# Optimization experiments

Measured on AMD Instinct MI355X. Metric: run time of the kernel, lower is better.

Reference implementation:

```python
import jax, jax.numpy as jnp
import numpy as np

B, T, H, M = 64, 1024, 512, 256  # batch, max_time, out_dim(=annot_dim), memory_dim


def setup_inputs() -> dict:
    key = jax.random.key(0)
    ks = jax.random.split(key, 13)
    s = lambda k, shape, scale=1.0: jax.random.normal(k, shape, dtype=jnp.float32) * scale
    return {
        "memory": s(ks[0], (B, M)),
        "context": s(ks[1], (B, H)),
        "rnn_state": s(ks[2], (B, H)),
        "annotations": s(ks[3], (B, T, H)),
        "W_ih": s(ks[4], (3 * H, H + M), 0.04),
        "b_ih": s(ks[5], (3 * H,), 0.04),
        "W_hh": s(ks[6], (3 * H, H), 0.04),
        "b_hh": s(ks[7], (3 * H,), 0.04),
        "Wq": s(ks[8], (H, H), 0.04),
        "bq": s(ks[9], (H,), 0.04),
        "Wa": s(ks[10], (H, H), 0.04),
        "ba": s(ks[11], (H,), 0.04),
        "v": s(ks[12], (H,), 0.04),
    }


def reference(memory, context, rnn_state, annotations,
              W_ih, b_ih, W_hh, b_hh, Wq, bq, Wa, ba, v):
    # --- GRUCell step (torch semantics) ---
    x = jnp.concatenate([memory, context], axis=-1)          # (B, M+H)
    gi = x @ W_ih.T + b_ih                                   # (B, 3H)
    gh = rnn_state @ W_hh.T + b_hh                           # (B, 3H)
    i_r, i_z, i_n = jnp.split(gi, 3, axis=-1)
    h_r, h_z, h_n = jnp.split(gh, 3, axis=-1)
    r = jax.nn.sigmoid(i_r + h_r)
    z = jax.nn.sigmoid(i_z + h_z)
    n = jnp.tanh(i_n + r * h_n)
    h_new = (1.0 - z) * n + z * rnn_state                    # (B, H)

    # --- Bahdanau additive attention ---
    pq = h_new @ Wq.T + bq                                   # (B, H)
    pa = annotations @ Wa.T + ba                             # (B, T, H)
    scores = jnp.tanh(pq[:, None, :] + pa) @ v               # (B, T)
    align = jax.nn.softmax(scores, axis=-1)                  # (B, T)
    ctx = jnp.einsum('bt,btd->bd', align, annotations)       # (B, H)
    return (h_new, ctx, align)
```

## Files before the change

kernel.cpp:

```cpp
#include <hip/hip_runtime.h>
#include <hip/hip_bf16.h>


typedef __attribute__((ext_vector_type(8))) __bf16 bf16x8;
typedef __attribute__((ext_vector_type(8))) unsigned short u16x8;
typedef __attribute__((ext_vector_type(4))) float f32x4;
typedef __attribute__((ext_vector_type(4))) float f4v;

__device__ __forceinline__ unsigned short f2bf(float f) {
    __hip_bfloat16 h = __float2bfloat16(f);
    return __builtin_bit_cast(unsigned short, h);
}
__device__ __forceinline__ float tanh_fast(float x) {
    float e = __expf(2.0f * x);
    return 1.0f - 2.0f / (e + 1.0f);
}
__device__ __forceinline__ float sigmoid_f(float x) {
    return 1.0f / (1.0f + __expf(-x));
}
__device__ __forceinline__ int swz(int x) { return x ^ (((x >> 8) & 7) << 4); }
__device__ __forceinline__ f4v ntload4(const float* p) {
    return __builtin_nontemporal_load((const f4v*)p);
}

__global__ __launch_bounds__(256) void wconv_kernel(
    const float* __restrict__ W_ih, const float* __restrict__ W_hh,
    const float* __restrict__ Wq, const float* __restrict__ Wa,
    unsigned short* __restrict__ WihB, unsigned short* __restrict__ WhhB,
    unsigned short* __restrict__ WqB, unsigned short* __restrict__ WaB)
{
    const int cb = blockIdx.x * 4 + (threadIdx.x >> 6);
    const int l = threadIdx.x & 63;
    const float* src;
    unsigned short* dst;
    int K, local, NB, kt;
    if (cb < 2304) {
        src = W_ih; dst = WihB; K = 768; local = cb;
        NB = local / 24; kt = local % 24;
    } else if (cb < 3840) {
        src = W_hh; dst = WhhB; K = 512; local = cb - 2304;
        NB = local >> 4; kt = local & 15;
    } else if (cb < 4352) {
        src = Wq; dst = WqB; K = 512; local = cb - 3840;
        NB = local >> 4; kt = local & 15;
    } else {
        src = Wa; dst = WaB; K = 512; local = cb - 4352;
        NB = local >> 4; kt = local & 15;
    }
    const float* s = src + (size_t)(NB * 16 + (l & 15)) * K + kt * 32 + (l >> 4) * 8;
    float4 f0 = *(const float4*)s;
    float4 f1 = *(const float4*)(s + 4);
    u16x8 p;
    p[0] = f2bf(f0.x); p[1] = f2bf(f0.y); p[2] = f2bf(f0.z); p[3] = f2bf(f0.w);
    p[4] = f2bf(f1.x); p[5] = f2bf(f1.y); p[6] = f2bf(f1.z); p[7] = f2bf(f1.w);
    *(u16x8*)&dst[(size_t)local * 512 + l * 8] = p;
}

#define CVT8(f0, f1, AF)                                                           \
    {                                                                              \
        u16x8 p_;                                                                  \
        p_[0] = f2bf((f0).x); p_[1] = f2bf((f0).y); p_[2] = f2bf((f0).z); p_[3] = f2bf((f0).w); \
        p_[4] = f2bf((f1).x); p_[5] = f2bf((f1).y); p_[6] = f2bf((f1).z); p_[7] = f2bf((f1).w); \
        AF = __builtin_bit_cast(bf16x8, p_);                                       \
    }

__global__ __launch_bounds__(64) void gru_kernel(
    const float* __restrict__ memory, const float* __restrict__ context,
    const float* __restrict__ rnn_state,
    const unsigned short* __restrict__ WihB, const float* __restrict__ b_ih,
    const unsigned short* __restrict__ WhhB, const float* __restrict__ b_hh,
    float* __restrict__ h_new)
{
    const int l = threadIdx.x;
    const int mt = blockIdx.x >> 5;
    const int hb = blockIdx.x & 31;
    const int r = l & 15, g = l >> 4;
    const int row = mt * 16 + r;

    f32x4 a_ir = {0,0,0,0}, a_iz = {0,0,0,0}, a_in = {0,0,0,0};
    f32x4 a_hr = {0,0,0,0}, a_hz = {0,0,0,0}, a_hn = {0,0,0,0};

#pragma unroll
    for (int kt = 0; kt < 8; ++kt) {
        const float* s = memory + (size_t)row * 256 + kt * 32 + g * 8;
        float4 f0 = *(const float4*)s, f1 = *(const float4*)(s + 4);
        bf16x8 af; CVT8(f0, f1, af);
        bf16x8 b0 = __builtin_bit_cast(bf16x8, *(const u16x8*)&WihB[((size_t)(hb) * 24 + kt) * 512 + l * 8]);
        bf16x8 b1 = __builtin_bit_cast(bf16x8, *(const u16x8*)&WihB[((size_t)(32 + hb) * 24 + kt) * 512 + l * 8]);
        bf16x8 b2 = __builtin_bit_cast(bf16x8, *(const u16x8*)&WihB[((size_t)(64 + hb) * 24 + kt) * 512 + l * 8]);
        a_ir = __builtin_amdgcn_mfma_f32_16x16x32_bf16(af, b0, a_ir, 0, 0, 0);
        a_iz = __builtin_amdgcn_mfma_f32_16x16x32_bf16(af, b1, a_iz, 0, 0, 0);
        a_in = __builtin_amdgcn_mfma_f32_16x16x32_bf16(af, b2, a_in, 0, 0, 0);
    }
#pragma unroll
    for (int kt = 8; kt < 24; ++kt) {
        const float* s = context + (size_t)row * 512 + (kt - 8) * 32 + g * 8;
        float4 f0 = *(const float4*)s, f1 = *(const float4*)(s + 4);
        bf16x8 af; CVT8(f0, f1, af);
        bf16x8 b0 = __builtin_bit_cast(bf16x8, *(const u16x8*)&WihB[((size_t)(hb) * 24 + kt) * 512 + l * 8]);
        bf16x8 b1 = __builtin_bit_cast(bf16x8, *(const u16x8*)&WihB[((size_t)(32 + hb) * 24 + kt) * 512 + l * 8]);
        bf16x8 b2 = __builtin_bit_cast(bf16x8, *(const u16x8*)&WihB[((size_t)(64 + hb) * 24 + kt) * 512 + l * 8]);
        a_ir = __builtin_amdgcn_mfma_f32_16x16x32_bf16(af, b0, a_ir, 0, 0, 0);
        a_iz = __builtin_amdgcn_mfma_f32_16x16x32_bf16(af, b1, a_iz, 0, 0, 0);
        a_in = __builtin_amdgcn_mfma_f32_16x16x32_bf16(af, b2, a_in, 0, 0, 0);
    }
#pragma unroll
    for (int kt = 0; kt < 16; ++kt) {
        const float* s = rnn_state + (size_t)row * 512 + kt * 32 + g * 8;
        float4 f0 = *(const float4*)s, f1 = *(const float4*)(s + 4);
        bf16x8 af; CVT8(f0, f1, af);
        bf16x8 b0 = __builtin_bit_cast(bf16x8, *(const u16x8*)&WhhB[((size_t)(hb) * 16 + kt) * 512 + l * 8]);
        bf16x8 b1 = __builtin_bit_cast(bf16x8, *(const u16x8*)&WhhB[((size_t)(32 + hb) * 16 + kt) * 512 + l * 8]);
        bf16x8 b2 = __builtin_bit_cast(bf16x8, *(const u16x8*)&WhhB[((size_t)(64 + hb) * 16 + kt) * 512 + l * 8]);
        a_hr = __builtin_amdgcn_mfma_f32_16x16x32_bf16(af, b0, a_hr, 0, 0, 0);
        a_hz = __builtin_amdgcn_mfma_f32_16x16x32_bf16(af, b1, a_hz, 0, 0, 0);
        a_hn = __builtin_amdgcn_mfma_f32_16x16x32_bf16(af, b2, a_hn, 0, 0, 0);
    }
    const int c = hb * 16 + r;
    const float bir = b_ih[c], biz = b_ih[512 + c], bin = b_ih[1024 + c];
    const float bhr = b_hh[c], bhz = b_hh[512 + c], bhn = b_hh[1024 + c];
#pragma unroll
    for (int r2 = 0; r2 < 4; ++r2) {
        const int m = mt * 16 + g * 4 + r2;
        float rr = sigmoid_f(a_ir[r2] + bir + a_hr[r2] + bhr);
        float zz = sigmoid_f(a_iz[r2] + biz + a_hz[r2] + bhz);
        float nn = tanh_fast(a_in[r2] + bin + rr * (a_hn[r2] + bhn));
        float h0 = rnn_state[(size_t)m * 512 + c];
        h_new[(size_t)m * 512 + c] = (1.f - zz) * nn + zz * h0;
    }
}

__global__ __launch_bounds__(64) void pq_kernel(
    const float* __restrict__ h_new, const unsigned short* __restrict__ WqB,
    const float* __restrict__ bq, const float* __restrict__ ba,
    float* __restrict__ q)
{
    const int l = threadIdx.x;
    const int mt = blockIdx.x >> 5;
    const int hb = blockIdx.x & 31;
    const int r = l & 15, g = l >> 4;
    const int row = mt * 16 + r;
    f32x4 acc = {0,0,0,0};
#pragma unroll
    for (int kt = 0; kt < 16; ++kt) {
        const float* s = h_new + (size_t)row * 512 + kt * 32 + g * 8;
        float4 f0 = *(const float4*)s, f1 = *(const float4*)(s + 4);
        bf16x8 af; CVT8(f0, f1, af);
        bf16x8 b0 = __builtin_bit_cast(bf16x8, *(const u16x8*)&WqB[((size_t)hb * 16 + kt) * 512 + l * 8]);
        acc = __builtin_amdgcn_mfma_f32_16x16x32_bf16(af, b0, acc, 0, 0, 0);
    }
    const int c = hb * 16 + r;
    const float add = bq[c] + ba[c];
#pragma unroll
    for (int r2 = 0; r2 < 4; ++r2)
        q[(size_t)(mt * 16 + g * 4 + r2) * 512 + c] = acc[r2] + add;
}

__global__ __launch_bounds__(512, 2) void scores_kernel(
    const float* __restrict__ ann, const unsigned short* __restrict__ WaB,
    const float* __restrict__ qv, const float* __restrict__ v,
    float* __restrict__ scores)
{
    __shared__ unsigned short As[65536];
    __shared__ float s_sc[128];
    const int tid = threadIdx.x;
    const int l = tid & 63;
    const int w = tid >> 6;
    const int wr = w >> 2;
    const int wc = w & 3;
    const int r0 = blockIdx.x * 128;
    const int b = blockIdx.x >> 3;

    if (tid < 128) s_sc[tid] = 0.f;

#pragma unroll
    for (int p = 0; p < 16; ++p) {
        int cidx = tid + p * 512;
        int row = cidx >> 6;
        int c8 = cidx & 63;
        int kt = c8 >> 2, g = c8 & 3;
        int rtg = row >> 4, r15 = row & 15;
        const float* s = ann + (size_t)(r0 + row) * 512 + c8 * 8;
        f4v f0 = ntload4(s);
        f4v f1 = ntload4(s + 4);
        u16x8 pk;
        pk[0] = f2bf(f0[0]); pk[1] = f2bf(f0[1]); pk[2] = f2bf(f0[2]); pk[3] = f2bf(f0[3]);
        pk[4] = f2bf(f1[0]); pk[5] = f2bf(f1[1]); pk[6] = f2bf(f1[2]); pk[7] = f2bf(f1[3]);
        int logical = (((rtg * 16 + kt) * 64) + g * 16 + r15) * 16;
        *(u16x8*)((char*)As + swz(logical)) = pk;
    }
    __syncthreads();

    f32x4 acc[4][8];
#pragma unroll
    for (int i = 0; i < 4; ++i)
#pragma unroll
        for (int j = 0; j < 8; ++j) acc[i][j] = (f32x4){0.f, 0.f, 0.f, 0.f};

#define LOADB(BV, ktv)                                                                 \
    {                                                                                  \
        _Pragma("unroll")                                                              \
        for (int ct_ = 0; ct_ < 8; ++ct_)                                              \
            BV[ct_] = *(const u16x8*)(WaB +                                            \
                ((size_t)((wc * 8 + ct_) * 16 + (ktv))) * 512 + l * 8);                \
    }

#define MFMA_K(ktv, BV)                                                                \
    {                                                                                  \
        _Pragma("unroll")                                                              \
        for (int rt_ = 0; rt_ < 4; ++rt_) {                                            \
            int logical = (((wr * 4 + rt_) * 16 + (ktv)) * 64 + l) * 16;               \
            bf16x8 af_ = __builtin_bit_cast(bf16x8,                                    \
                *(const u16x8*)((char*)As + swz(logical)));                            \
            _Pragma("unroll")                                                          \
            for (int ct_ = 0; ct_ < 8; ++ct_)                                          \
                acc[rt_][ct_] = __builtin_amdgcn_mfma_f32_16x16x32_bf16(               \
                    af_, __builtin_bit_cast(bf16x8, BV[ct_]), acc[rt_][ct_], 0, 0, 0); \
        }                                                                              \
    }

    u16x8 bvE[8], bvO[8];
    LOADB(bvE, 0);
    for (int kt2 = 0; kt2 < 8; ++kt2) {
        LOADB(bvO, 2 * kt2 + 1);
        MFMA_K(2 * kt2, bvE);
        if (kt2 < 7) LOADB(bvE, 2 * kt2 + 2);
        MFMA_K(2 * kt2 + 1, bvO);
    }
#undef LOADB
#undef MFMA_K

    float rsum[4][4];
#pragma unroll
    for (int i = 0; i < 4; ++i)
#pragma unroll
        for (int j = 0; j < 4; ++j) rsum[i][j] = 0.f;

#pragma unroll
    for (int ct = 0; ct < 8; ++ct) {
        int col = wc * 128 + ct * 16 + (l & 15);
        float qq = qv[b * 512 + col];
        float vv = v[col];
#pragma unroll
        for (int rt = 0; rt < 4; ++rt) {
            f32x4 a = acc[rt][ct];
#pragma unroll
            for (int r2 = 0; r2 < 4; ++r2)
                rsum[rt][r2] += tanh_fast(a[r2] + qq) * vv;
        }
    }
#pragma unroll
    for (int m = 1; m < 16; m <<= 1) {
#pragma unroll
        for (int rt = 0; rt < 4; ++rt)
#pragma unroll
            for (int r2 = 0; r2 < 4; ++r2)
                rsum[rt][r2] += __shfl_xor(rsum[rt][r2], m, 64);
    }
    if ((l & 15) == 0) {
        int g = l >> 4;
#pragma unroll
        for (int rt = 0; rt < 4; ++rt)
#pragma unroll
            for (int r2 = 0; r2 < 4; ++r2)
                atomicAdd(&s_sc[wr * 64 + rt * 16 + g * 4 + r2], rsum[rt][r2]);
    }
    __syncthreads();
    if (tid < 128) scores[r0 + tid] = s_sc[tid];
}

__global__ __launch_bounds__(256) void softmax_kernel(
    const float* __restrict__ scores, float* __restrict__ align_)
{
    const int b = blockIdx.x, tid = threadIdx.x;
    __shared__ float red[256];
    float s[4];
#pragma unroll
    for (int j = 0; j < 4; ++j) s[j] = scores[b * 1024 + j * 256 + tid];
    float mx = fmaxf(fmaxf(s[0], s[1]), fmaxf(s[2], s[3]));
    red[tid] = mx; __syncthreads();
    for (int off = 128; off > 0; off >>= 1) {
        if (tid < off) red[tid] = fmaxf(red[tid], red[tid + off]);
        __syncthreads();
    }
    mx = red[0]; __syncthreads();
    float e[4], sum = 0.f;
#pragma unroll
    for (int j = 0; j < 4; ++j) { e[j] = __expf(s[j] - mx); sum += e[j]; }
    red[tid] = sum; __syncthreads();
    for (int off = 128; off > 0; off >>= 1) {
        if (tid < off) red[tid] += red[tid + off];
        __syncthreads();
    }
    float inv = 1.0f / red[0];
#pragma unroll
    for (int j = 0; j < 4; ++j) align_[b * 1024 + j * 256 + tid] = e[j] * inv;
}

__global__ __launch_bounds__(256) void ctx_part_kernel(
    const float* __restrict__ ann, const float* __restrict__ align_,
    float* __restrict__ part)
{
    const int tid = threadIdx.x;
    const int b = blockIdx.x;
    const int tc = blockIdx.y;
    __shared__ float al[128];
    __shared__ float4 red[128];
    if (tid < 128) al[tid] = align_[b * 1024 + tc * 128 + tid];
    __syncthreads();
    const int rp = tid >> 7, d4 = (tid & 127) * 4;
    const float* ap = ann + ((size_t)(b * 1024 + tc * 128)) * 512 + d4;
    float4 acc = {0.f, 0.f, 0.f, 0.f};
    for (int tt = rp; tt < 128; tt += 2) {
        float4 x = *(const float4*)(ap + (size_t)tt * 512);
        float wv = al[tt];
        acc.x += wv * x.x; acc.y += wv * x.y; acc.z += wv * x.z; acc.w += wv * x.w;
    }
    if (rp == 1) red[tid & 127] = acc;
    __syncthreads();
    if (rp == 0) {
        float4 o = red[tid];
        o.x += acc.x; o.y += acc.y; o.z += acc.z; o.w += acc.w;
        *(float4*)&part[((size_t)(tc * 64 + b)) * 512 + d4] = o;
    }
}

__global__ __launch_bounds__(256) void ctx_reduce_kernel(
    const float* __restrict__ part, float* __restrict__ ctx)
{
    int i4 = (blockIdx.x * 256 + threadIdx.x) * 4;
    float4 s = {0.f, 0.f, 0.f, 0.f};
#pragma unroll
    for (int p = 0; p < 8; ++p) {
        float4 x = *(const float4*)&part[(size_t)p * 32768 + i4];
        s.x += x.x; s.y += x.y; s.z += x.z; s.w += x.w;
    }
    *(float4*)&ctx[i4] = s;
}

extern "C" void kernel_launch(void* const* d_in, const int* in_sizes, int n_in,
                              void* d_out, int out_size, void* d_ws, size_t ws_size,
                              hipStream_t stream)
{
    (void)in_sizes; (void)n_in; (void)out_size; (void)ws_size;
    const float* memory    = (const float*)d_in[0];
    const float* context   = (const float*)d_in[1];
    const float* rnn_state = (const float*)d_in[2];
    const float* ann       = (const float*)d_in[3];
    const float* W_ih      = (const float*)d_in[4];
    const float* b_ih      = (const float*)d_in[5];
    const float* W_hh      = (const float*)d_in[6];
    const float* b_hh      = (const float*)d_in[7];
    const float* Wq        = (const float*)d_in[8];
    const float* bq        = (const float*)d_in[9];
    const float* Wa        = (const float*)d_in[10];
    const float* ba        = (const float*)d_in[11];
    const float* v         = (const float*)d_in[12];

    float* out    = (float*)d_out;
    float* h_new  = out;
    float* ctx    = out + 32768;
    float* align_ = out + 65536;

    char* wsb = (char*)d_ws;
    float* q    = (float*)(wsb + 0);
    float* sc   = (float*)(wsb + 131072);
    float* part = (float*)(wsb + 393216);
    unsigned short* WihB = (unsigned short*)(wsb + 1441792);
    unsigned short* WhhB = (unsigned short*)(wsb + 3801088);
    unsigned short* WqB  = (unsigned short*)(wsb + 5373952);
    unsigned short* WaB  = (unsigned short*)(wsb + 5898240);

    wconv_kernel<<<dim3(1216), dim3(256), 0, stream>>>(
        W_ih, W_hh, Wq, Wa, WihB, WhhB, WqB, WaB);
    gru_kernel<<<dim3(128), dim3(64), 0, stream>>>(
        memory, context, rnn_state, WihB, b_ih, WhhB, b_hh, h_new);
    pq_kernel<<<dim3(128), dim3(64), 0, stream>>>(h_new, WqB, bq, ba, q);
    scores_kernel<<<dim3(512), dim3(512), 0, stream>>>(ann, WaB, q, v, sc);
    softmax_kernel<<<dim3(64), dim3(256), 0, stream>>>(sc, align_);
    ctx_part_kernel<<<dim3(64, 8), dim3(256), 0, stream>>>(ann, align_, part);
    ctx_reduce_kernel<<<dim3(32), dim3(256), 0, stream>>>(part, ctx);
}
```

Baseline: 130.2 us.

## Stage Wa slice in LDS and stream annotations from registers in scores kernel

The scores kernel now splits the output columns into four 128-column slices per block. Each block loads its Wa slice into LDS once with global_load_lds, and each wave streams its 64 annotation rows directly from global memory into registers, converting them to bf16 on the fly. Partial scores for each column slice go to a 4x workspace buffer, and the softmax kernel adds them up, which replaces the shared-memory atomics. The cost is that annotations are read four times, once per column slice, in exchange for Wa staying resident in LDS. The grid also shrinks to 256 blocks, each handling two 512-row passes.

```diff
diff --git a/kernel.cpp b/kernel.cpp
--- a/kernel.cpp
+++ b/kernel.cpp
@@ -5,7 +5,6 @@
 typedef __attribute__((ext_vector_type(8))) __bf16 bf16x8;
 typedef __attribute__((ext_vector_type(8))) unsigned short u16x8;
 typedef __attribute__((ext_vector_type(4))) float f32x4;
-typedef __attribute__((ext_vector_type(4))) float f4v;
 
 __device__ __forceinline__ unsigned short f2bf(float f) {
     __hip_bfloat16 h = __float2bfloat16(f);
@@ -17,10 +16,6 @@
 }
 __device__ __forceinline__ float sigmoid_f(float x) {
     return 1.0f / (1.0f + __expf(-x));
-}
-__device__ __forceinline__ int swz(int x) { return x ^ (((x >> 8) & 7) << 4); }
-__device__ __forceinline__ f4v ntload4(const float* p) {
-    return __builtin_nontemporal_load((const f4v*)p);
 }
 
 __global__ __launch_bounds__(256) void wconv_kernel(
@@ -159,124 +154,123 @@
 __global__ __launch_bounds__(512, 2) void scores_kernel(
     const float* __restrict__ ann, const unsigned short* __restrict__ WaB,
     const float* __restrict__ qv, const float* __restrict__ v,
-    float* __restrict__ scores)
-{
-    __shared__ unsigned short As[65536];
-    __shared__ float s_sc[128];
+    float* __restrict__ sc4)
+{
+    __shared__ unsigned short Bs[65536];
     const int tid = threadIdx.x;
     const int l = tid & 63;
     const int w = tid >> 6;
-    const int wr = w >> 2;
-    const int wc = w & 3;
-    const int r0 = blockIdx.x * 128;
-    const int b = blockIdx.x >> 3;
-
-    if (tid < 128) s_sc[tid] = 0.f;
+    const int bid = blockIdx.x;
+    const int cs = (bid >> 3) & 3;
+    const int rg = ((bid >> 5) << 3) | (bid & 7);
 
 #pragma unroll
     for (int p = 0; p < 16; ++p) {
-        int cidx = tid + p * 512;
-        int row = cidx >> 6;
-        int c8 = cidx & 63;
-        int kt = c8 >> 2, g = c8 & 3;
-        int rtg = row >> 4, r15 = row & 15;
-        const float* s = ann + (size_t)(r0 + row) * 512 + c8 * 8;
-        f4v f0 = ntload4(s);
-        f4v f1 = ntload4(s + 4);
-        u16x8 pk;
-        pk[0] = f2bf(f0[0]); pk[1] = f2bf(f0[1]); pk[2] = f2bf(f0[2]); pk[3] = f2bf(f0[3]);
-        pk[4] = f2bf(f1[0]); pk[5] = f2bf(f1[1]); pk[6] = f2bf(f1[2]); pk[7] = f2bf(f1[3]);
-        int logical = (((rtg * 16 + kt) * 64) + g * 16 + r15) * 16;
-        *(u16x8*)((char*)As + swz(logical)) = pk;
+        int chunk = w + p * 8;
+        const unsigned short* gsrc =
+            WaB + ((size_t)((cs * 8 + (chunk >> 4)) * 16 + (chunk & 15))) * 512 + l * 8;
+        unsigned short* ldst = &Bs[chunk * 512 + l * 8];
+        __builtin_amdgcn_global_load_lds(
+            (const __attribute__((address_space(1))) unsigned int*)gsrc,
+            (__attribute__((address_space(3))) unsigned int*)ldst, 16, 0, 0);
     }
     __syncthreads();
 
-    f32x4 acc[4][8];
-#pragma unroll
-    for (int i = 0; i < 4; ++i)
-#pragma unroll
-        for (int j = 0; j < 8; ++j) acc[i][j] = (f32x4){0.f, 0.f, 0.f, 0.f};
-
-#define LOADB(BV, ktv)                                                                 \
-    {                                                                                  \
-        _Pragma("unroll")                                                              \
-        for (int ct_ = 0; ct_ < 8; ++ct_)                                              \
-            BV[ct_] = *(const u16x8*)(WaB +                                            \
-                ((size_t)((wc * 8 + ct_) * 16 + (ktv))) * 512 + l * 8);                \
-    }
-
-#define MFMA_K(ktv, BV)                                                                \
+#define LOADA(AR, ktv)                                                                 \
     {                                                                                  \
         _Pragma("unroll")                                                              \
         for (int rt_ = 0; rt_ < 4; ++rt_) {                                            \
-            int logical = (((wr * 4 + rt_) * 16 + (ktv)) * 64 + l) * 16;               \
-            bf16x8 af_ = __builtin_bit_cast(bf16x8,                                    \
-                *(const u16x8*)((char*)As + swz(logical)));                            \
+            const float* s_ = abase + (size_t)rt_ * (16 * 512) + (ktv) * 32;           \
+            AR[rt_][0] = *(const float4*)s_;                                           \
+            AR[rt_][1] = *(const float4*)(s_ + 4);                                     \
+        }                                                                              \
+    }
+
+#define MFMA_K(AR, ktv)                                                                \
+    {                                                                                  \
+        _Pragma("unroll")                                                              \
+        for (int rt_ = 0; rt_ < 4; ++rt_) {                                            \
+            bf16x8 af_; CVT8(AR[rt_][0], AR[rt_][1], af_);                             \
             _Pragma("unroll")                                                          \
-            for (int ct_ = 0; ct_ < 8; ++ct_)                                          \
+            for (int ct_ = 0; ct_ < 8; ++ct_) {                                        \
+                bf16x8 bf_ = __builtin_bit_cast(bf16x8,                                \
+                    *(const u16x8*)&Bs[(ct_ * 16 + (ktv)) * 512 + l * 8]);             \
                 acc[rt_][ct_] = __builtin_amdgcn_mfma_f32_16x16x32_bf16(               \
-                    af_, __builtin_bit_cast(bf16x8, BV[ct_]), acc[rt_][ct_], 0, 0, 0); \
+                    af_, bf_, acc[rt_][ct_], 0, 0, 0);                                 \
+            }                                                                          \
         }                                                                              \
     }
 
-    u16x8 bvE[8], bvO[8];
-    LOADB(bvE, 0);
-    for (int kt2 = 0; kt2 < 8; ++kt2) {
-        LOADB(bvO, 2 * kt2 + 1);
-        MFMA_K(2 * kt2, bvE);
-        if (kt2 < 7) LOADB(bvE, 2 * kt2 + 2);
-        MFMA_K(2 * kt2 + 1, bvO);
-    }
-#undef LOADB
+    for (int p2 = 0; p2 < 2; ++p2) {
+        const int row_base = rg * 1024 + p2 * 512 + w * 64;
+        const float* abase = ann + (size_t)(row_base + (l & 15)) * 512 + (l >> 4) * 8;
+
+        f32x4 acc[4][8];
+#pragma unroll
+        for (int i = 0; i < 4; ++i)
+#pragma unroll
+            for (int j = 0; j < 8; ++j) acc[i][j] = (f32x4){0.f, 0.f, 0.f, 0.f};
+
+        float4 aE[4][2], aO[4][2];
+        LOADA(aE, 0);
+        for (int kt2 = 0; kt2 < 8; ++kt2) {
+            LOADA(aO, 2 * kt2 + 1);
+            MFMA_K(aE, 2 * kt2);
+            if (kt2 < 7) LOADA(aE, 2 * kt2 + 2);
+            MFMA_K(aO, 2 * kt2 + 1);
+        }
+
+        float rsum[4][4];
+#pragma unroll
+        for (int i = 0; i < 4; ++i)
+#pragma unroll
+            for (int j = 0; j < 4; ++j) rsum[i][j] = 0.f;
+
+#pragma unroll
+        for (int ct = 0; ct < 8; ++ct) {
+            int col = cs * 128 + ct * 16 + (l & 15);
+            float qq = qv[rg * 512 + col];
+            float vv = v[col];
+#pragma unroll
+            for (int rt = 0; rt < 4; ++rt) {
+                f32x4 a = acc[rt][ct];
+#pragma unroll
+                for (int r2 = 0; r2 < 4; ++r2)
+                    rsum[rt][r2] += tanh_fast(a[r2] + qq) * vv;
+            }
+        }
+#pragma unroll
+        for (int m = 1; m < 16; m <<= 1) {
+#pragma unroll
+            for (int rt = 0; rt < 4; ++rt)
+#pragma unroll
+                for (int r2 = 0; r2 < 4; ++r2)
+                    rsum[rt][r2] += __shfl_xor(rsum[rt][r2], m, 64);
+        }
+        if ((l & 15) == 0) {
+            int g = l >> 4;
+#pragma unroll
+            for (int rt = 0; rt < 4; ++rt)
+#pragma unroll
+                for (int r2 = 0; r2 < 4; ++r2)
+                    sc4[(size_t)cs * 65536 + row_base + rt * 16 + g * 4 + r2] = rsum[rt][r2];
+        }
+    }
+#undef LOADA
 #undef MFMA_K
-
-    float rsum[4][4];
-#pragma unroll
-    for (int i = 0; i < 4; ++i)
-#pragma unroll
-        for (int j = 0; j < 4; ++j) rsum[i][j] = 0.f;
-
-#pragma unroll
-    for (int ct = 0; ct < 8; ++ct) {
-        int col = wc * 128 + ct * 16 + (l & 15);
-        float qq = qv[b * 512 + col];
-        float vv = v[col];
-#pragma unroll
-        for (int rt = 0; rt < 4; ++rt) {
-            f32x4 a = acc[rt][ct];
-#pragma unroll
-            for (int r2 = 0; r2 < 4; ++r2)
-                rsum[rt][r2] += tanh_fast(a[r2] + qq) * vv;
-        }
-    }
-#pragma unroll
-    for (int m = 1; m < 16; m <<= 1) {
-#pragma unroll
-        for (int rt = 0; rt < 4; ++rt)
-#pragma unroll
-            for (int r2 = 0; r2 < 4; ++r2)
-                rsum[rt][r2] += __shfl_xor(rsum[rt][r2], m, 64);
-    }
-    if ((l & 15) == 0) {
-        int g = l >> 4;
-#pragma unroll
-        for (int rt = 0; rt < 4; ++rt)
-#pragma unroll
-            for (int r2 = 0; r2 < 4; ++r2)
-                atomicAdd(&s_sc[wr * 64 + rt * 16 + g * 4 + r2], rsum[rt][r2]);
-    }
-    __syncthreads();
-    if (tid < 128) scores[r0 + tid] = s_sc[tid];
 }
 
 __global__ __launch_bounds__(256) void softmax_kernel(
-    const float* __restrict__ scores, float* __restrict__ align_)
+    const float* __restrict__ sc4, float* __restrict__ align_)
 {
     const int b = blockIdx.x, tid = threadIdx.x;
     __shared__ float red[256];
     float s[4];
 #pragma unroll
-    for (int j = 0; j < 4; ++j) s[j] = scores[b * 1024 + j * 256 + tid];
+    for (int j = 0; j < 4; ++j) {
+        int r = b * 1024 + j * 256 + tid;
+        s[j] = sc4[r] + sc4[65536 + r] + sc4[131072 + r] + sc4[196608 + r];
+    }
     float mx = fmaxf(fmaxf(s[0], s[1]), fmaxf(s[2], s[3]));
     red[tid] = mx; __syncthreads();
     for (int off = 128; off > 0; off >>= 1) {
@@ -364,20 +358,20 @@
 
     char* wsb = (char*)d_ws;
     float* q    = (float*)(wsb + 0);
-    float* sc   = (float*)(wsb + 131072);
-    float* part = (float*)(wsb + 393216);
-    unsigned short* WihB = (unsigned short*)(wsb + 1441792);
-    unsigned short* WhhB = (unsigned short*)(wsb + 3801088);
-    unsigned short* WqB  = (unsigned short*)(wsb + 5373952);
-    unsigned short* WaB  = (unsigned short*)(wsb + 5898240);
+    float* sc4  = (float*)(wsb + 131072);
+    float* part = (float*)(wsb + 1179648);
+    unsigned short* WihB = (unsigned short*)(wsb + 2228224);
+    unsigned short* WhhB = (unsigned short*)(wsb + 4587520);
+    unsigned short* WqB  = (unsigned short*)(wsb + 6160384);
+    unsigned short* WaB  = (unsigned short*)(wsb + 6684672);
 
     wconv_kernel<<<dim3(1216), dim3(256), 0, stream>>>(
         W_ih, W_hh, Wq, Wa, WihB, WhhB, WqB, WaB);
     gru_kernel<<<dim3(128), dim3(64), 0, stream>>>(
         memory, context, rnn_state, WihB, b_ih, WhhB, b_hh, h_new);
     pq_kernel<<<dim3(128), dim3(64), 0, stream>>>(h_new, WqB, bq, ba, q);
-    scores_kernel<<<dim3(512), dim3(512), 0, stream>>>(ann, WaB, q, v, sc);
-    softmax_kernel<<<dim3(64), dim3(256), 0, stream>>>(sc, align_);
+    scores_kernel<<<dim3(256), dim3(512), 0, stream>>>(ann, WaB, q, v, sc4);
+    softmax_kernel<<<dim3(64), dim3(256), 0, stream>>>(sc4, align_);
     ctx_part_kernel<<<dim3(64, 8), dim3(256), 0, stream>>>(ann, align_, part);
     ctx_reduce_kernel<<<dim3(32), dim3(256), 0, stream>>>(part, ctx);
 }
```

Result: slower. 142.4 us (+9.3%).
